# Kernel tuning notes

Hardware: AMD Instinct MI355X
Metric: run time of the kernel (lower is better)

The kernel has to match this reference:

```python
import jax, jax.numpy as jnp
import numpy as np

N = 30000
N_CONTEXT = 32
IN_FEAT = 256
HIDDEN = 128
ALPHA = 0.2
NEG_INF = -9e15


def setup_inputs() -> dict:
    key = jax.random.key(0)
    k1, k2, k3, k4, k5, k6, k7 = jax.random.split(key, 7)
    h_i = jax.random.normal(k1, (N, IN_FEAT), dtype=jnp.float32)
    idx = jax.random.randint(k2, (N, N_CONTEXT), 0, N)
    pad = jax.random.uniform(k3, (N, N_CONTEXT)) < 0.1
    context_indices = jnp.where(pad, -1, idx)
    s_in = 1.0 / np.sqrt(IN_FEAT)
    s_h = 1.0 / np.sqrt(2 * HIDDEN)
    W_i = jax.random.uniform(k4, (IN_FEAT, HIDDEN), minval=-s_in, maxval=s_in, dtype=jnp.float32)
    W_j = jax.random.uniform(k5, (IN_FEAT, HIDDEN), minval=-s_in, maxval=s_in, dtype=jnp.float32)
    a_w = jax.random.uniform(k6, (2 * HIDDEN,), minval=-s_h, maxval=s_h, dtype=jnp.float32)
    a_b = jax.random.uniform(k7, (), minval=-s_h, maxval=s_h, dtype=jnp.float32)
    return {"h_i": h_i, "context_indices": context_indices,
            "W_i": W_i, "W_j": W_j, "a_w": a_w, "a_b": a_b}


def reference(h_i, context_indices, W_i, W_j, a_w, a_b):
    # Pad with a zero-feature row; index -1 hits the last row (same as torch cat trick).
    h_padded = jnp.concatenate([h_i, jnp.zeros((1, h_i.shape[1]), h_i.dtype)], axis=0)
    h_j = h_padded[context_indices]                       # [N, C, F] gather
    Wh_i = h_i @ W_i                                      # [N, H]
    Wh_j = jnp.einsum('ncf,fh->nch', h_j, W_j)            # [N, C, H]
    # attention_layer(cat(Wh_i, Wh_j)) split into two dot products + bias
    scores = (Wh_i @ a_w[:HIDDEN])[:, None] + Wh_j @ a_w[HIDDEN:] + a_b  # [N, C]
    scores = jnp.where(scores >= 0, scores, ALPHA * scores)              # leaky relu
    scores = jnp.where(context_indices >= 0, scores, NEG_INF)
    attn = jax.nn.softmax(scores, axis=1)                 # [N, C]
    h_prime = jnp.einsum('nc,nch->nh', attn, Wh_j)        # [N, H]
    return h_prime
```

## Files before the change

### kernel.cpp

```cpp
#include <hip/hip_runtime.h>

#define NN   30000
#define NCTX 32
#define FIN  256
#define HID  128

typedef short short8 __attribute__((ext_vector_type(8)));
typedef float f32x4  __attribute__((ext_vector_type(4)));
typedef _Float16 half2v __attribute__((ext_vector_type(2)));

#define SEL_LO 0x01000504u
#define SEL_HI 0x03020706u

__device__ __forceinline__ unsigned short f2b(float x) {
    union { float f; unsigned u; } v; v.f = x;
    unsigned r = v.u + 0x7FFFu + ((v.u >> 16) & 1u);
    return (unsigned short)(r >> 16);
}
__device__ __forceinline__ unsigned short f2b_trunc(float x) {
    union { float f; unsigned u; } v; v.f = x;
    return (unsigned short)(v.u >> 16);
}
__device__ __forceinline__ float b2f(unsigned short u) {
    union { unsigned u; float f; } v; v.u = ((unsigned)u) << 16;
    return v.f;
}
__device__ __forceinline__ unsigned short f2h(float x) {
    const _Float16 h = (_Float16)x;
    return __builtin_bit_cast(unsigned short, h);
}
__device__ __forceinline__ float dot2(unsigned vp, unsigned wp, float acc) {
    return __builtin_amdgcn_fdot2(__builtin_bit_cast(half2v, vp),
                                  __builtin_bit_cast(half2v, wp), acc, false);
}

__global__ __launch_bounds__(64) void k_pack(const float* __restrict__ Wj,
                                             const float* __restrict__ Wi,
                                             const float* __restrict__ aw,
                                             short8* __restrict__ whi,
                                             short8* __restrict__ wlo,
                                             float* __restrict__ vi) {
    const int b = blockIdx.x;
    const int l = threadIdx.x;
    if (b >= 64) {
        const int fi = l >> 4;
        const int q  = l & 15;
        const int f  = (b - 64) * 4 + fi;
        const float4 w0 = *(const float4*)(Wi + (long)f * HID + q * 8);
        const float4 w1 = *(const float4*)(Wi + (long)f * HID + q * 8 + 4);
        const float4 a0 = *(const float4*)(aw + q * 8);
        const float4 a1 = *(const float4*)(aw + q * 8 + 4);
        float s = w0.x * a0.x + w0.y * a0.y + w0.z * a0.z + w0.w * a0.w
                + w1.x * a1.x + w1.y * a1.y + w1.z * a1.z + w1.w * a1.w;
        s += __shfl_xor(s, 1); s += __shfl_xor(s, 2);
        s += __shfl_xor(s, 4); s += __shfl_xor(s, 8);
        if (q == 0) vi[f] = s;
        return;
    }
    const int s = b >> 3, t = b & 7;
    const int kbase = s * 32 + (l >> 4) * 8;
    const int c = t * 16 + (l & 15);
    short8 hi, lo;
    #pragma unroll
    for (int j = 0; j < 8; ++j) {
        const float w = Wj[(long)(kbase + j) * HID + c];
        const unsigned short h = f2b_trunc(w);
        hi[j] = (short)h;
        lo[j] = (short)f2b(w - b2f(h));
    }
    whi[b * 64 + l] = hi;
    wlo[b * 64 + l] = lo;
}

__global__ __launch_bounds__(256) void k_gemm(const float* __restrict__ hin,
                                              const short8* __restrict__ whi,
                                              const short8* __restrict__ wlo,
                                              const float* __restrict__ vi,
                                              const float* __restrict__ aw,
                                              const float* __restrict__ ab,
                                              unsigned short* __restrict__ Wh,
                                              float* __restrict__ sib,
                                              float* __restrict__ sjv) {
    const int tid  = threadIdx.x;
    const int l    = tid & 63;
    const int wave = blockIdx.x * 4 + (tid >> 6);
    if (wave >= NN / 16) return;
    const long rowbase = (long)wave * 16;
    const int r  = l & 15;
    const int kg = l >> 4;

    const float* hrow = hin + (rowbase + r) * FIN + kg * 8;
    const float* vip  = vi + kg * 8;

    f32x4 acc[8];
    #pragma unroll
    for (int t = 0; t < 8; ++t) acc[t] = (f32x4){0.f, 0.f, 0.f, 0.f};
    float si = 0.f;

    #pragma unroll
    for (int s = 0; s < 8; ++s) {
        short8 BH[8], BL[8];
        #pragma unroll
        for (int t = 0; t < 8; ++t) {
            BH[t] = whi[(s * 8 + t) * 64 + l];
            BL[t] = wlo[(s * 8 + t) * 64 + l];
        }
        const float4 ha = *(const float4*)(hrow + s * 32);
        const float4 hb = *(const float4*)(hrow + s * 32 + 4);
        const float4 va = *(const float4*)(vip + s * 32);
        const float4 vb = *(const float4*)(vip + s * 32 + 4);
        const float hv[8] = {ha.x, ha.y, ha.z, ha.w, hb.x, hb.y, hb.z, hb.w};
        const float vv[8] = {va.x, va.y, va.z, va.w, vb.x, vb.y, vb.z, vb.w};
        short8 ahi, alo;
        #pragma unroll
        for (int j = 0; j < 8; ++j) {
            si += hv[j] * vv[j];
            const unsigned short hb16 = f2b_trunc(hv[j]);
            ahi[j] = (short)hb16;
            alo[j] = (short)f2b(hv[j] - b2f(hb16));
        }
        #pragma unroll
        for (int t = 0; t < 8; ++t) {
            acc[t] = __builtin_amdgcn_mfma_f32_16x16x32_bf16(ahi, BH[t], acc[t], 0, 0, 0);
            acc[t] = __builtin_amdgcn_mfma_f32_16x16x32_bf16(alo, BH[t], acc[t], 0, 0, 0);
            acc[t] = __builtin_amdgcn_mfma_f32_16x16x32_bf16(ahi, BL[t], acc[t], 0, 0, 0);
        }
    }

    si += __shfl_xor(si, 16);
    si += __shfl_xor(si, 32);
    if (l < 16) sib[rowbase + l] = si + ab[0];

    float aw2v[8];
    #pragma unroll
    for (int t = 0; t < 8; ++t) aw2v[t] = aw[HID + t * 16 + r];
    #pragma unroll
    for (int j = 0; j < 4; ++j) {
        float p = 0.f;
        #pragma unroll
        for (int t = 0; t < 8; ++t) p += acc[t][j] * aw2v[t];
        p += __shfl_xor(p, 1); p += __shfl_xor(p, 2);
        p += __shfl_xor(p, 4); p += __shfl_xor(p, 8);
        if (r == 0) sjv[rowbase + kg * 4 + j] = p;
    }

    #pragma unroll
    for (int j = 0; j < 4; ++j) {
        const long rr = rowbase + kg * 4 + j;
        #pragma unroll
        for (int t = 0; t < 8; ++t)
            Wh[rr * HID + t * 16 + r] = f2h(acc[t][j]);
    }
}

__global__ __launch_bounds__(256) void k_attn(const int* __restrict__ ctx,
                                              const unsigned short* __restrict__ Wh,
                                              const float* __restrict__ sib,
                                              const float* __restrict__ sjv,
                                              float* __restrict__ out) {
    const int lane = threadIdx.x & 63;
    const long n = (long)blockIdx.x * 4 + (threadIdx.x >> 6);
    const int c = lane & 31;
    const int idx = ctx[n * NCTX + c];
    const int icl = (idx >= 0) ? idx : 0;
    float s;
    if (idx >= 0) {
        s = sib[n] + sjv[icl];
        s = (s >= 0.f) ? s : 0.2f * s;
    } else {
        s = -9e15f;
    }
    float mx = s;
    #pragma unroll
    for (int m = 16; m >= 1; m >>= 1) mx = fmaxf(mx, __shfl_xor(mx, m));
    const float e = __expf(s - mx);
    float sum = e;
    #pragma unroll
    for (int m = 16; m >= 1; m >>= 1) sum += __shfl_xor(sum, m);
    const float at = (idx >= 0) ? e / sum : 0.f;

    const int q  = lane >> 4;
    const unsigned coff = (lane & 15) * 16;
    const char* base = (const char*)Wh;

    float a[8] = {0.f,0.f,0.f,0.f,0.f,0.f,0.f,0.f};
    #pragma unroll
    for (int p = 0; p < 4; ++p) {
        const float wA = __shfl(at,  p * 8 + q);
        const int   iA = __shfl(icl, p * 8 + q);
        const float wB = __shfl(at,  p * 8 + 4 + q);
        const int   iB = __shfl(icl, p * 8 + 4 + q);
        const uint4 uA = *(const uint4*)(base + (((unsigned)iA << 8) | coff));
        const uint4 uB = *(const uint4*)(base + (((unsigned)iB << 8) | coff));
        const unsigned hA = (unsigned)f2h(wA);
        const unsigned hB = (unsigned)f2h(wB);
        const unsigned wp = __builtin_amdgcn_perm(hA, hB, SEL_LO);
        a[0] = dot2(__builtin_amdgcn_perm(uA.x, uB.x, SEL_LO), wp, a[0]);
        a[1] = dot2(__builtin_amdgcn_perm(uA.x, uB.x, SEL_HI), wp, a[1]);
        a[2] = dot2(__builtin_amdgcn_perm(uA.y, uB.y, SEL_LO), wp, a[2]);
        a[3] = dot2(__builtin_amdgcn_perm(uA.y, uB.y, SEL_HI), wp, a[3]);
        a[4] = dot2(__builtin_amdgcn_perm(uA.z, uB.z, SEL_LO), wp, a[4]);
        a[5] = dot2(__builtin_amdgcn_perm(uA.z, uB.z, SEL_HI), wp, a[5]);
        a[6] = dot2(__builtin_amdgcn_perm(uA.w, uB.w, SEL_LO), wp, a[6]);
        a[7] = dot2(__builtin_amdgcn_perm(uA.w, uB.w, SEL_HI), wp, a[7]);
    }
    #pragma unroll
    for (int i = 0; i < 8; ++i) {
        a[i] += __shfl_xor(a[i], 16);
        a[i] += __shfl_xor(a[i], 32);
    }
    if (lane < 16) {
        float4* op = (float4*)(out + n * HID + (coff >> 2) * 2);
        op[0] = (float4){a[0], a[1], a[2], a[3]};
        op[1] = (float4){a[4], a[5], a[6], a[7]};
    }
}

extern "C" void kernel_launch(void* const* d_in, const int* in_sizes, int n_in,
                              void* d_out, int out_size, void* d_ws, size_t ws_size,
                              hipStream_t stream) {
    const float* h_i = (const float*)d_in[0];
    const int*   ctx = (const int*)d_in[1];
    const float* W_i = (const float*)d_in[2];
    const float* W_j = (const float*)d_in[3];
    const float* a_w = (const float*)d_in[4];
    const float* a_b = (const float*)d_in[5];
    float* out = (float*)d_out;

    char* ws = (char*)d_ws;
    unsigned short* Wh = (unsigned short*)ws;
    float* sib = (float*)(ws + 7680000);
    float* sjv = (float*)(ws + 7800000);
    float* vi  = (float*)(ws + 7920000);
    short8* whi = (short8*)(ws + 7921024);
    short8* wlo = (short8*)(ws + 7986560);

    k_pack<<<128, 64, 0, stream>>>(W_j, W_i, a_w, whi, wlo, vi);
    k_gemm<<<(NN / 16 + 3) / 4, 256, 0, stream>>>(h_i, whi, wlo, vi, a_w, a_b, Wh, sib, sjv);
    k_attn<<<NN / 4, 256, 0, stream>>>(ctx, Wh, sib, sjv, out);
}
```

Measured before the change: 52.90 us.

## Split Wh table into column halves and gather in two cache-resident passes

The GEMM now writes the fp16 Wh table as two separate 64-column halves, each 3.84 MB. The attention kernel runs twice, once per half, so the random row gathers hit a smaller working set that should fit in L2/LLC. Each block also prefetches a slice of its half-table at the start to warm the cache. The cost is recomputing the softmax and rereading the context indices twice, plus an extra kernel launch.

Result: slower. 58.96 us (+11.4%).

```diff
diff --git a/kernel.cpp b/kernel.cpp
--- a/kernel.cpp
+++ b/kernel.cpp
@@ -4,6 +4,7 @@
 #define NCTX 32
 #define FIN  256
 #define HID  128
+#define HTBL 3840000
 
 typedef short short8 __attribute__((ext_vector_type(8)));
 typedef float f32x4  __attribute__((ext_vector_type(4)));
@@ -78,7 +79,8 @@
                                               const float* __restrict__ vi,
                                               const float* __restrict__ aw,
                                               const float* __restrict__ ab,
-                                              unsigned short* __restrict__ Wh,
+                                              unsigned short* __restrict__ Wh0,
+                                              unsigned short* __restrict__ Wh1,
                                               float* __restrict__ sib,
                                               float* __restrict__ sjv) {
     const int tid  = threadIdx.x;
@@ -148,19 +150,39 @@
     for (int j = 0; j < 4; ++j) {
         const long rr = rowbase + kg * 4 + j;
         #pragma unroll
-        for (int t = 0; t < 8; ++t)
-            Wh[rr * HID + t * 16 + r] = f2h(acc[t][j]);
-    }
-}
-
-__global__ __launch_bounds__(256) void k_attn(const int* __restrict__ ctx,
-                                              const unsigned short* __restrict__ Wh,
-                                              const float* __restrict__ sib,
-                                              const float* __restrict__ sjv,
-                                              float* __restrict__ out) {
-    const int lane = threadIdx.x & 63;
-    const long n = (long)blockIdx.x * 4 + (threadIdx.x >> 6);
-    const int c = lane & 31;
+        for (int t = 0; t < 4; ++t)
+            Wh0[rr * 64 + t * 16 + r] = f2h(acc[t][j]);
+        #pragma unroll
+        for (int t = 4; t < 8; ++t)
+            Wh1[rr * 64 + (t - 4) * 16 + r] = f2h(acc[t][j]);
+    }
+}
+
+__global__ __launch_bounds__(256) void k_attn_half(const int* __restrict__ ctx,
+                                                   const unsigned short* __restrict__ Whp,
+                                                   const float* __restrict__ sib,
+                                                   const float* __restrict__ sjv,
+                                                   float* __restrict__ out,
+                                                   int p) {
+    const int tid  = threadIdx.x;
+    const int lane = tid & 63;
+
+    {
+        const char* wb = (const char*)Whp;
+        const long o1 = (long)(blockIdx.x >> 3) * 8192 + tid * 16;
+        const long o2 = o1 + 4096;
+        unsigned k1 = 0, k2 = 0;
+        if (o1 < HTBL) k1 = ((const uint4*)(wb + o1))->x;
+        if (o2 < HTBL) k2 = ((const uint4*)(wb + o2))->x;
+        asm volatile("" :: "v"(k1), "v"(k2));
+    }
+
+    const int wid  = tid >> 6;
+    const long nb  = (long)blockIdx.x * 8 + wid * 2;
+    const int h    = lane >> 5;
+    const long n   = nb + h;
+    const int c    = lane & 31;
+
     const int idx = ctx[n * NCTX + c];
     const int icl = (idx >= 0) ? idx : 0;
     float s;
@@ -179,19 +201,21 @@
     for (int m = 16; m >= 1; m >>= 1) sum += __shfl_xor(sum, m);
     const float at = (idx >= 0) ? e / sum : 0.f;
 
-    const int q  = lane >> 4;
-    const unsigned coff = (lane & 15) * 16;
-    const char* base = (const char*)Wh;
+    const int r  = (lane >> 3) & 3;
+    const int cl = lane & 7;
+    const char* base = (const char*)Whp;
 
     float a[8] = {0.f,0.f,0.f,0.f,0.f,0.f,0.f,0.f};
     #pragma unroll
-    for (int p = 0; p < 4; ++p) {
-        const float wA = __shfl(at,  p * 8 + q);
-        const int   iA = __shfl(icl, p * 8 + q);
-        const float wB = __shfl(at,  p * 8 + 4 + q);
-        const int   iB = __shfl(icl, p * 8 + 4 + q);
-        const uint4 uA = *(const uint4*)(base + (((unsigned)iA << 8) | coff));
-        const uint4 uB = *(const uint4*)(base + (((unsigned)iB << 8) | coff));
+    for (int pp = 0; pp < 4; ++pp) {
+        const int srcA = (lane & 32) | (pp * 8 + r);
+        const int srcB = (lane & 32) | (pp * 8 + 4 + r);
+        const float wA = __shfl(at,  srcA);
+        const int   iA = __shfl(icl, srcA);
+        const float wB = __shfl(at,  srcB);
+        const int   iB = __shfl(icl, srcB);
+        const uint4 uA = *(const uint4*)(base + (((unsigned)iA << 7) | (cl << 4)));
+        const uint4 uB = *(const uint4*)(base + (((unsigned)iB << 7) | (cl << 4)));
         const unsigned hA = (unsigned)f2h(wA);
         const unsigned hB = (unsigned)f2h(wB);
         const unsigned wp = __builtin_amdgcn_perm(hA, hB, SEL_LO);
@@ -206,11 +230,11 @@
     }
     #pragma unroll
     for (int i = 0; i < 8; ++i) {
+        a[i] += __shfl_xor(a[i], 8);
         a[i] += __shfl_xor(a[i], 16);
-        a[i] += __shfl_xor(a[i], 32);
-    }
-    if (lane < 16) {
-        float4* op = (float4*)(out + n * HID + (coff >> 2) * 2);
+    }
+    if (r == 0) {
+        float4* op = (float4*)(out + n * HID + p * 64 + cl * 8);
         op[0] = (float4){a[0], a[1], a[2], a[3]};
         op[1] = (float4){a[4], a[5], a[6], a[7]};
     }
@@ -228,7 +252,8 @@
     float* out = (float*)d_out;
 
     char* ws = (char*)d_ws;
-    unsigned short* Wh = (unsigned short*)ws;
+    unsigned short* Wh0 = (unsigned short*)ws;
+    unsigned short* Wh1 = (unsigned short*)(ws + HTBL);
     float* sib = (float*)(ws + 7680000);
     float* sjv = (float*)(ws + 7800000);
     float* vi  = (float*)(ws + 7920000);
@@ -236,6 +261,8 @@
     short8* wlo = (short8*)(ws + 7986560);
 
     k_pack<<<128, 64, 0, stream>>>(W_j, W_i, a_w, whi, wlo, vi);
-    k_gemm<<<(NN / 16 + 3) / 4, 256, 0, stream>>>(h_i, whi, wlo, vi, a_w, a_b, Wh, sib, sjv);
-    k_attn<<<NN / 4, 256, 0, stream>>>(ctx, Wh, sib, sjv, out);
-}
+    k_gemm<<<(NN / 16 + 3) / 4, 256, 0, stream>>>(h_i, whi, wlo, vi, a_w, a_b,
+                                                  Wh0, Wh1, sib, sjv);
+    k_attn_half<<<NN / 8, 256, 0, stream>>>(ctx, Wh0, sib, sjv, out, 0);
+    k_attn_half<<<NN / 8, 256, 0, stream>>>(ctx, Wh1, sib, sjv, out, 1);
+}
```
